# Kernel optimization log

Hardware: AMD Instinct MI355X
Metric: run time of the kernel (lower is better)

The kernel has to match this reference:

```python
import jax, jax.numpy as jnp
import numpy as np

HIDDEN = 1024
B, S = 32, 2048
MASKED_BIAS = -10000.0


def setup_inputs() -> dict:
    key = jax.random.key(0)
    ks = jax.random.split(key, 10)
    scale = 1.0 / np.sqrt(HIDDEN)
    inp = {
        "h": jax.random.normal(ks[0], (B, HIDDEN), jnp.float32),
        "K": jax.random.normal(ks[1], (B, S, HIDDEN), jnp.float32),
        "cov": jax.random.uniform(ks[2], (B, S), jnp.float32),
        "mask": jax.random.bernoulli(ks[3], 0.1, (B, S)).astype(jnp.float32),
        # parameters (PyTorch Linear: y = x @ W.T + b)
        "W_h": jax.random.uniform(ks[4], (HIDDEN, HIDDEN), jnp.float32, -scale, scale),
        "b_h": jnp.zeros((HIDDEN,), jnp.float32),
        "W_K": jax.random.uniform(ks[5], (HIDDEN, HIDDEN), jnp.float32, -scale, scale),
        "b_K": jnp.zeros((HIDDEN,), jnp.float32),
        "W_cov": jax.random.uniform(ks[6], (HIDDEN, 1), jnp.float32, -1.0, 1.0),
        "b_cov": jnp.zeros((HIDDEN,), jnp.float32),
        "W_v": jax.random.uniform(ks[7], (1, HIDDEN), jnp.float32, -scale, scale),
        "b_v": jnp.zeros((1,), jnp.float32),
    }
    return inp


def reference(h, K, cov, mask, W_h, b_h, W_K, b_K, W_cov, b_cov, W_v, b_v):
    # h_l: (B, 1, H); K_l: (B, S, H); c_l: (B, S, H)
    h_l = (h @ W_h.T + b_h)[:, None, :]
    K_l = jnp.einsum("bsh,gh->bsg", K, W_K) + b_K
    c_l = cov[:, :, None] * W_cov[:, 0] + b_cov  # linear_cov on scalar cov
    t = jnp.tanh(h_l + K_l + c_l)                 # (B, S, H)
    e = jnp.einsum("bsh,h->bs", t, W_v[0]) + b_v[0]
    e = e + mask * MASKED_BIAS
    a = jax.nn.softmax(e, axis=-1)                # (B, S)
    out = jnp.einsum("bs,bsh->bh", a, K)          # context vector
    cov_new = cov + a
    return (out, a, cov_new)
```

## Files before the change

kernel.cpp:

```cpp
#include <hip/hip_runtime.h>
#include <hip/hip_bf16.h>

#define HIDDEN 1024
#define B_SZ 32
#define S_SZ 2048
#define M_TOT (B_SZ * S_SZ)
#define MASKED_BIAS -10000.0f

using bf16   = __bf16;
using bf16x4 = __attribute__((ext_vector_type(4))) __bf16;
using bf16x8 = __attribute__((ext_vector_type(8))) __bf16;
using f32x4  = __attribute__((ext_vector_type(4))) float;

__device__ __forceinline__ float tanh_fast(float x) {
    float xc = fminf(fmaxf(x, -15.f), 15.f);
    float e2 = __expf(2.f * xc);
    return (e2 - 1.f) * __frcp_rn(e2 + 1.f);
}

__global__ __launch_bounds__(256) void k_wconv(
    const float* __restrict__ W, bf16* __restrict__ out)
{
    int i = blockIdx.x * 256 + threadIdx.x;
    const float4* p = (const float4*)W + (size_t)i * 2;
    float4 a = p[0], b = p[1];
    bf16x8 v = { (bf16)a.x, (bf16)a.y, (bf16)a.z, (bf16)a.w,
                 (bf16)b.x, (bf16)b.y, (bf16)b.z, (bf16)b.w };
    *(bf16x8*)(out + (size_t)i * 8) = v;
}

__global__ __launch_bounds__(256) void k_kconv(
    const float* __restrict__ K, bf16* __restrict__ out)
{
    size_t i = (size_t)blockIdx.x * 256 + threadIdx.x;
    const float4* p = (const float4*)K + i * 2;
    float4 a = p[0], b = p[1];
    bf16x8 v = { (bf16)a.x, (bf16)a.y, (bf16)a.z, (bf16)a.w,
                 (bf16)b.x, (bf16)b.y, (bf16)b.z, (bf16)b.w };
    *(bf16x8*)(out + i * 8) = v;
}

__global__ __launch_bounds__(256) void k_hlplus(
    const float* __restrict__ h, const float* __restrict__ W_h,
    const float* __restrict__ b_h, const float* __restrict__ b_K,
    const float* __restrict__ b_cov, float* __restrict__ hl_plus)
{
    int wid  = blockIdx.x * 4 + (threadIdx.x >> 6);
    int lane = threadIdx.x & 63;
    int b = wid & 31;
    int g = wid >> 5;
    const float4* hv = (const float4*)(h + b * HIDDEN);
    const float4* wv = (const float4*)(W_h + g * HIDDEN);
    float acc = 0.f;
#pragma unroll
    for (int i = 0; i < 4; ++i) {
        float4 a = hv[i * 64 + lane];
        float4 w = wv[i * 64 + lane];
        acc += a.x * w.x + a.y * w.y + a.z * w.z + a.w * w.w;
    }
#pragma unroll
    for (int off = 32; off; off >>= 1) acc += __shfl_xor(acc, off);
    if (lane == 0)
        hl_plus[b * HIDDEN + g] = acc + b_h[g] + b_K[g] + b_cov[g];
}

#define NT_N 4

__global__ __launch_bounds__(512) void k_fused_g(
    const bf16*  __restrict__ Kbf,
    const bf16*  __restrict__ Bbf,
    const float* __restrict__ hl_plus,
    const float* __restrict__ W_cov,
    const float* __restrict__ cov,
    const float* __restrict__ W_v,
    float* __restrict__ e_part)
{
    __shared__ __align__(16) bf16 AsT[2][2][256][32];
    __shared__ __align__(16) bf16 BsT[2][2][256][32];
    __shared__ float e_buf[256][4];

    const int tid = threadIdx.x;
    const int bid = blockIdx.x;
    const int lid = (bid & 7) * 128 + (bid >> 3);
    const int mt  = lid >> 2;
    const int nt  = lid & 3;
    const int row0 = mt * 256;
    const int col0 = nt * 256;

    const int w    = tid >> 6;
    const int lane = tid & 63;
    const int wr   = w >> 2;
    const int wc   = w & 3;
    const int lr   = lane & 15;
    const int kb   = lane >> 4;
    const int wrB  = wr * 128;
    const int wcB  = wc * 64;
    const int colA = (kb ^ ((lr >> 1) & 3)) * 8;

    const int srow = lane >> 2;
    const int gch  = (lane & 3) ^ ((lane >> 3) & 3);
    const bf16* Abase = Kbf + (size_t)(row0 + w * 32 + srow) * HIDDEN + gch * 8;
    const bf16* Bbase = Bbf + (size_t)(col0 + w * 32 + srow) * HIDDEN + gch * 8;

    f32x4 acc[8][4] = {};

#define STAGE(KT, H, D)                                                   \
    _Pragma("unroll") for (int j = 0; j < 2; ++j) {                       \
        __builtin_amdgcn_global_load_lds(                                 \
            (const __attribute__((address_space(1))) void*)               \
                (Abase + (size_t)j * 16 * HIDDEN + (KT) * 64 + (H) * 32), \
            (__attribute__((address_space(3))) void*)                     \
                &AsT[D][H][w * 32 + j * 16][0], 16, 0, 0);                \
        __builtin_amdgcn_global_load_lds(                                 \
            (const __attribute__((address_space(1))) void*)               \
                (Bbase + (size_t)j * 16 * HIDDEN + (KT) * 64 + (H) * 32), \
            (__attribute__((address_space(3))) void*)                     \
                &BsT[D][H][w * 32 + j * 16][0], 16, 0, 0);                \
    }

#define RD_A(D, H, MP)                                                   \
    _Pragma("unroll") for (int j = 0; j < 4; ++j)                        \
        afr[j] = *(const bf16x8*)                                        \
            &AsT[D][H][wrB + (MP) * 64 + j * 16 + lr][colA];

#define RD_B(D, H)                                                       \
    _Pragma("unroll") for (int n = 0; n < 4; ++n)                        \
        bfr[n] = *(const bf16x8*)&BsT[D][H][wcB + n * 16 + lr][colA];

#define MFMA16(MP)                                                       \
    __builtin_amdgcn_s_setprio(1);                                       \
    _Pragma("unroll") for (int j = 0; j < 4; ++j)                        \
        _Pragma("unroll") for (int n = 0; n < 4; ++n)                    \
            acc[(MP) * 4 + j][n] = __builtin_amdgcn_mfma_f32_16x16x32_bf16( \
                afr[j], bfr[n], acc[(MP) * 4 + j][n], 0, 0, 0);          \
    __builtin_amdgcn_s_setprio(0);

#define MEMBAR() asm volatile("" ::: "memory")
#define LGKM0()  asm volatile("s_waitcnt lgkmcnt(0)" ::: "memory")
#define VM(n)    asm volatile("s_waitcnt vmcnt(" #n ")" ::: "memory")
#define SBAR()   __builtin_amdgcn_s_barrier()
#define P_OPEN()  MEMBAR(); SBAR(); LGKM0();
#define P_CLOSE() MEMBAR(); SBAR();

#define TILE_STEADY(D, KT_NEXT)                                          \
    {                                                                    \
        bf16x8 afr[4], bfr[4];                                           \
        RD_B(D, 0) RD_A(D, 0, 0) STAGE(KT_NEXT, 0, D ^ 1)                \
        P_OPEN() MFMA16(0) P_CLOSE()                                     \
        RD_A(D, 0, 1)                                                    \
        P_OPEN() MFMA16(1) VM(4); P_CLOSE()                              \
        RD_B(D, 1) RD_A(D, 1, 0) STAGE(KT_NEXT, 1, D ^ 1)                \
        P_OPEN() MFMA16(0) P_CLOSE()                                     \
        RD_A(D, 1, 1)                                                    \
        P_OPEN() MFMA16(1) VM(4); P_CLOSE()                              \
    }

#define TILE_LAST(D)                                                     \
    {                                                                    \
        bf16x8 afr[4], bfr[4];                                           \
        RD_B(D, 0) RD_A(D, 0, 0)                                         \
        P_OPEN() MFMA16(0) P_CLOSE()                                     \
        RD_A(D, 0, 1)                                                    \
        P_OPEN() MFMA16(1) VM(0); P_CLOSE()                              \
        RD_B(D, 1) RD_A(D, 1, 0)                                         \
        P_OPEN() MFMA16(0) P_CLOSE()                                     \
        RD_A(D, 1, 1)                                                    \
        P_OPEN() MFMA16(1) P_CLOSE()                                     \
    }

    STAGE(0, 0, 0)
    STAGE(0, 1, 0)
    VM(4);
    MEMBAR(); SBAR();

    for (int kt2 = 0; kt2 < 7; ++kt2) {
        TILE_STEADY(0, 2 * kt2 + 1)
        TILE_STEADY(1, 2 * kt2 + 2)
    }
    TILE_STEADY(0, 15)
    TILE_LAST(1)

    const int bidx = row0 >> 11;
    float hlv[4], wcv[4], wvv[4];
#pragma unroll
    for (int n = 0; n < 4; ++n) {
        int g = col0 + wcB + n * 16 + lr;
        hlv[n] = hl_plus[bidx * HIDDEN + g];
        wcv[n] = W_cov[g];
        wvv[n] = W_v[g];
    }
#pragma unroll
    for (int am = 0; am < 8; ++am) {
#pragma unroll
        for (int i = 0; i < 4; ++i) {
            int rloc = wrB + am * 16 + kb * 4 + i;
            float cv = cov[row0 + rloc];
            float ep = 0.f;
#pragma unroll
            for (int n = 0; n < 4; ++n) {
                float arg = acc[am][n][i] + hlv[n] + cv * wcv[n];
                ep += tanh_fast(arg) * wvv[n];
            }
            ep += __shfl_xor(ep, 1);
            ep += __shfl_xor(ep, 2);
            ep += __shfl_xor(ep, 4);
            ep += __shfl_xor(ep, 8);
            if (lr == 0) e_buf[rloc][wc] = ep;
        }
    }
    __syncthreads();
    if (tid < 256)
        e_part[(size_t)nt * M_TOT + row0 + tid] =
            e_buf[tid][0] + e_buf[tid][1] + e_buf[tid][2] + e_buf[tid][3];

#undef STAGE
#undef RD_A
#undef RD_B
#undef MFMA16
#undef TILE_STEADY
#undef TILE_LAST
#undef MEMBAR
#undef LGKM0
#undef VM
#undef SBAR
#undef P_OPEN
#undef P_CLOSE
}

__global__ __launch_bounds__(256) void k_softmax(
    const float* __restrict__ e_part, const float* __restrict__ mask,
    const float* __restrict__ cov, const float* __restrict__ b_v,
    float* __restrict__ a_out, float* __restrict__ cov_out)
{
    __shared__ float red[8];
    int b = blockIdx.x, tid = threadIdx.x;
    float bv = b_v[0];
    float ev[8];
    float mx = -1e30f;
#pragma unroll
    for (int j = 0; j < 8; ++j) {
        int s = j * 256 + tid;
        int idx = b * S_SZ + s;
        float e = bv;
#pragma unroll
        for (int p = 0; p < 4; ++p) e += e_part[(size_t)p * M_TOT + idx];
        e += mask[idx] * MASKED_BIAS;
        ev[j] = e;
        mx = fmaxf(mx, e);
    }
#pragma unroll
    for (int off = 32; off; off >>= 1) mx = fmaxf(mx, __shfl_xor(mx, off));
    if ((tid & 63) == 0) red[tid >> 6] = mx;
    __syncthreads();
    mx = fmaxf(fmaxf(red[0], red[1]), fmaxf(red[2], red[3]));
    float sum = 0.f;
#pragma unroll
    for (int j = 0; j < 8; ++j) { ev[j] = __expf(ev[j] - mx); sum += ev[j]; }
#pragma unroll
    for (int off = 32; off; off >>= 1) sum += __shfl_xor(sum, off);
    if ((tid & 63) == 0) red[4 + (tid >> 6)] = sum;
    __syncthreads();
    sum = red[4] + red[5] + red[6] + red[7];
    float inv = 1.f / sum;
#pragma unroll
    for (int j = 0; j < 8; ++j) {
        int idx = b * S_SZ + j * 256 + tid;
        float a = ev[j] * inv;
        a_out[idx]   = a;
        cov_out[idx] = cov[idx] + a;
    }
}

__global__ __launch_bounds__(256) void k_ctx_part_bf(
    const bf16* __restrict__ Kbf, const float* __restrict__ a_out,
    float* __restrict__ part_out)
{
    int sc = blockIdx.x;
    int b  = blockIdx.y;
    int tid = threadIdx.x;
    const bf16* Kb = Kbf + ((size_t)b * S_SZ + sc * 128) * HIDDEN;
    const float* ab = a_out + b * S_SZ + sc * 128;
    float4 acc = {0.f, 0.f, 0.f, 0.f};
#pragma unroll 4
    for (int s = 0; s < 128; ++s) {
        float av = ab[s];
        bf16x4 kv = *(const bf16x4*)(Kb + (size_t)s * HIDDEN + tid * 4);
        acc.x += av * (float)kv[0];
        acc.y += av * (float)kv[1];
        acc.z += av * (float)kv[2];
        acc.w += av * (float)kv[3];
    }
    ((float4*)part_out)[((size_t)b * 16 + sc) * 256 + tid] = acc;
}

__global__ __launch_bounds__(256) void k_ctx_reduce(
    const float* __restrict__ part_out, float* __restrict__ out, int nc)
{
    int b = blockIdx.x, tid = threadIdx.x;
    float4 acc = {0.f, 0.f, 0.f, 0.f};
    for (int sc = 0; sc < nc; ++sc) {
        float4 v = ((const float4*)part_out)[((size_t)b * nc + sc) * 256 + tid];
        acc.x += v.x; acc.y += v.y; acc.z += v.z; acc.w += v.w;
    }
    ((float4*)out)[b * 256 + tid] = acc;
}

extern "C" void kernel_launch(void* const* d_in, const int* in_sizes, int n_in,
                              void* d_out, int out_size, void* d_ws, size_t ws_size,
                              hipStream_t stream)
{
    const float* h     = (const float*)d_in[0];
    const float* Kin   = (const float*)d_in[1];
    const float* cov   = (const float*)d_in[2];
    const float* mask  = (const float*)d_in[3];
    const float* W_h   = (const float*)d_in[4];
    const float* b_h   = (const float*)d_in[5];
    const float* W_K   = (const float*)d_in[6];
    const float* b_K   = (const float*)d_in[7];
    const float* W_cov = (const float*)d_in[8];
    const float* b_cov = (const float*)d_in[9];
    const float* W_v   = (const float*)d_in[10];
    const float* b_v   = (const float*)d_in[11];

    float* out_ctx = (float*)d_out;
    float* a_out   = out_ctx + B_SZ * HIDDEN;
    float* cov_out = a_out + M_TOT;

    float* ws       = (float*)d_ws;
    float* hl_plus  = ws;
    float* e_part   = ws + 32768;
    float* part_out = e_part;
    bf16*  Bbf      = (bf16*)(e_part + 4 * M_TOT);
    bf16*  Kbf      = (bf16*)((char*)Bbf + (size_t)HIDDEN * HIDDEN * sizeof(bf16));

    k_wconv<<<512, 256, 0, stream>>>(W_K, Bbf);
    k_hlplus<<<8192, 256, 0, stream>>>(h, W_h, b_h, b_K, b_cov, hl_plus);
    k_kconv<<<(M_TOT * HIDDEN / 8) / 256, 256, 0, stream>>>(Kin, Kbf);
    k_fused_g<<<256 * NT_N, 512, 0, stream>>>(
        Kbf, Bbf, hl_plus, W_cov, cov, W_v, e_part);
    k_softmax<<<B_SZ, 256, 0, stream>>>(e_part, mask, cov, b_v, a_out, cov_out);
    dim3 g4(16, B_SZ);
    k_ctx_part_bf<<<g4, 256, 0, stream>>>(Kbf, a_out, part_out);
    k_ctx_reduce<<<B_SZ, 256, 0, stream>>>(part_out, out_ctx, 16);
}
```

Before: 320.1 us.

## Shrink GEMM N-tile to 128 with K-step 32 and simpler double buffering

Replaces the 256x256 tile GEMM, which used a hand-scheduled barrier and waitcnt pipeline, with a 256x128 tile at K-step 32. The new version uses plain double buffering with __syncthreads and a launch bound of 4 waves per SIMD. The aim is lower LDS and register use so more blocks can be resident and hide latency. In exchange the K activations are re-read from memory twice as many times, with 8 column partials instead of 4. It also loses the fine-grained MFMA/load interleaving and adds more partial-sum traffic into softmax.

```diff
diff --git a/kernel.cpp b/kernel.cpp
--- a/kernel.cpp
+++ b/kernel.cpp
@@ -64,9 +64,9 @@
         hl_plus[b * HIDDEN + g] = acc + b_h[g] + b_K[g] + b_cov[g];
 }
 
-#define NT_N 4
-
-__global__ __launch_bounds__(512) void k_fused_g(
+#define NT_N 8
+
+__global__ __launch_bounds__(512, 4) void k_fused8(
     const bf16*  __restrict__ Kbf,
     const bf16*  __restrict__ Bbf,
     const float* __restrict__ hl_plus,
@@ -75,17 +75,17 @@
     const float* __restrict__ W_v,
     float* __restrict__ e_part)
 {
-    __shared__ __align__(16) bf16 AsT[2][2][256][32];
-    __shared__ __align__(16) bf16 BsT[2][2][256][32];
+    __shared__ __align__(16) bf16 As[2][256][32];
+    __shared__ __align__(16) bf16 Bs[2][128][32];
     __shared__ float e_buf[256][4];
 
     const int tid = threadIdx.x;
     const int bid = blockIdx.x;
-    const int lid = (bid & 7) * 128 + (bid >> 3);
-    const int mt  = lid >> 2;
-    const int nt  = lid & 3;
+    const int lid = (bid & 7) * 256 + (bid >> 3);
+    const int mt  = lid >> 3;
+    const int nt  = lid & 7;
     const int row0 = mt * 256;
-    const int col0 = nt * 256;
+    const int col0 = nt * 128;
 
     const int w    = tid >> 6;
     const int lane = tid & 63;
@@ -93,112 +93,82 @@
     const int wc   = w & 3;
     const int lr   = lane & 15;
     const int kb   = lane >> 4;
-    const int wrB  = wr * 128;
-    const int wcB  = wc * 64;
     const int colA = (kb ^ ((lr >> 1) & 3)) * 8;
 
     const int srow = lane >> 2;
     const int gch  = (lane & 3) ^ ((lane >> 3) & 3);
-    const bf16* Abase = Kbf + (size_t)(row0 + w * 32 + srow) * HIDDEN + gch * 8;
-    const bf16* Bbase = Bbf + (size_t)(col0 + w * 32 + srow) * HIDDEN + gch * 8;
-
-    f32x4 acc[8][4] = {};
-
-#define STAGE(KT, H, D)                                                   \
-    _Pragma("unroll") for (int j = 0; j < 2; ++j) {                       \
-        __builtin_amdgcn_global_load_lds(                                 \
-            (const __attribute__((address_space(1))) void*)               \
-                (Abase + (size_t)j * 16 * HIDDEN + (KT) * 64 + (H) * 32), \
-            (__attribute__((address_space(3))) void*)                     \
-                &AsT[D][H][w * 32 + j * 16][0], 16, 0, 0);                \
-        __builtin_amdgcn_global_load_lds(                                 \
-            (const __attribute__((address_space(1))) void*)               \
-                (Bbase + (size_t)j * 16 * HIDDEN + (KT) * 64 + (H) * 32), \
-            (__attribute__((address_space(3))) void*)                     \
-                &BsT[D][H][w * 32 + j * 16][0], 16, 0, 0);                \
-    }
-
-#define RD_A(D, H, MP)                                                   \
-    _Pragma("unroll") for (int j = 0; j < 4; ++j)                        \
-        afr[j] = *(const bf16x8*)                                        \
-            &AsT[D][H][wrB + (MP) * 64 + j * 16 + lr][colA];
-
-#define RD_B(D, H)                                                       \
-    _Pragma("unroll") for (int n = 0; n < 4; ++n)                        \
-        bfr[n] = *(const bf16x8*)&BsT[D][H][wcB + n * 16 + lr][colA];
-
-#define MFMA16(MP)                                                       \
-    __builtin_amdgcn_s_setprio(1);                                       \
-    _Pragma("unroll") for (int j = 0; j < 4; ++j)                        \
-        _Pragma("unroll") for (int n = 0; n < 4; ++n)                    \
-            acc[(MP) * 4 + j][n] = __builtin_amdgcn_mfma_f32_16x16x32_bf16( \
-                afr[j], bfr[n], acc[(MP) * 4 + j][n], 0, 0, 0);          \
-    __builtin_amdgcn_s_setprio(0);
-
-#define MEMBAR() asm volatile("" ::: "memory")
-#define LGKM0()  asm volatile("s_waitcnt lgkmcnt(0)" ::: "memory")
-#define VM(n)    asm volatile("s_waitcnt vmcnt(" #n ")" ::: "memory")
-#define SBAR()   __builtin_amdgcn_s_barrier()
-#define P_OPEN()  MEMBAR(); SBAR(); LGKM0();
-#define P_CLOSE() MEMBAR(); SBAR();
-
-#define TILE_STEADY(D, KT_NEXT)                                          \
-    {                                                                    \
-        bf16x8 afr[4], bfr[4];                                           \
-        RD_B(D, 0) RD_A(D, 0, 0) STAGE(KT_NEXT, 0, D ^ 1)                \
-        P_OPEN() MFMA16(0) P_CLOSE()                                     \
-        RD_A(D, 0, 1)                                                    \
-        P_OPEN() MFMA16(1) VM(4); P_CLOSE()                              \
-        RD_B(D, 1) RD_A(D, 1, 0) STAGE(KT_NEXT, 1, D ^ 1)                \
-        P_OPEN() MFMA16(0) P_CLOSE()                                     \
-        RD_A(D, 1, 1)                                                    \
-        P_OPEN() MFMA16(1) VM(4); P_CLOSE()                              \
-    }
-
-#define TILE_LAST(D)                                                     \
-    {                                                                    \
-        bf16x8 afr[4], bfr[4];                                           \
-        RD_B(D, 0) RD_A(D, 0, 0)                                         \
-        P_OPEN() MFMA16(0) P_CLOSE()                                     \
-        RD_A(D, 0, 1)                                                    \
-        P_OPEN() MFMA16(1) VM(0); P_CLOSE()                              \
-        RD_B(D, 1) RD_A(D, 1, 0)                                         \
-        P_OPEN() MFMA16(0) P_CLOSE()                                     \
-        RD_A(D, 1, 1)                                                    \
-        P_OPEN() MFMA16(1) P_CLOSE()                                     \
-    }
-
-    STAGE(0, 0, 0)
-    STAGE(0, 1, 0)
-    VM(4);
-    MEMBAR(); SBAR();
-
-    for (int kt2 = 0; kt2 < 7; ++kt2) {
-        TILE_STEADY(0, 2 * kt2 + 1)
-        TILE_STEADY(1, 2 * kt2 + 2)
-    }
-    TILE_STEADY(0, 15)
-    TILE_LAST(1)
+    const bf16* Abase = Kbf + (size_t)(row0 + w * 16 + srow) * HIDDEN + gch * 8;
+    const bf16* Bbase = Bbf + (size_t)(col0 + w * 16 + srow) * HIDDEN + gch * 8;
+
+    f32x4 acc[8][2] = {};
+
+#define STAGE(KT, BUF)                                                    \
+    __builtin_amdgcn_global_load_lds(                                     \
+        (const __attribute__((address_space(1))) void*)(Abase + (KT) * 32),\
+        (__attribute__((address_space(3))) void*)&As[BUF][w * 16][0],     \
+        16, 0, 0);                                                        \
+    __builtin_amdgcn_global_load_lds(                                     \
+        (const __attribute__((address_space(1))) void*)                   \
+            (Abase + (size_t)128 * HIDDEN + (KT) * 32),                   \
+        (__attribute__((address_space(3))) void*)&As[BUF][128 + w * 16][0],\
+        16, 0, 0);                                                        \
+    __builtin_amdgcn_global_load_lds(                                     \
+        (const __attribute__((address_space(1))) void*)(Bbase + (KT) * 32),\
+        (__attribute__((address_space(3))) void*)&Bs[BUF][w * 16][0],     \
+        16, 0, 0);
+
+#define TILE_COMPUTE(BUF)                                                 \
+    {                                                                     \
+        bf16x8 afr[8], bfr[2];                                            \
+        _Pragma("unroll") for (int j = 0; j < 8; ++j)                     \
+            afr[j] = *(const bf16x8*)                                     \
+                &As[BUF][wr * 128 + j * 16 + lr][colA];                   \
+        _Pragma("unroll") for (int n = 0; n < 2; ++n)                     \
+            bfr[n] = *(const bf16x8*)&Bs[BUF][wc * 32 + n * 16 + lr][colA];\
+        __builtin_amdgcn_s_setprio(1);                                    \
+        _Pragma("unroll") for (int j = 0; j < 8; ++j)                     \
+            _Pragma("unroll") for (int n = 0; n < 2; ++n)                 \
+                acc[j][n] = __builtin_amdgcn_mfma_f32_16x16x32_bf16(      \
+                    afr[j], bfr[n], acc[j][n], 0, 0, 0);                  \
+        __builtin_amdgcn_s_setprio(0);                                    \
+    }
+
+    STAGE(0, 0)
+    __syncthreads();
+
+    for (int i = 0; i < 15; ++i) {
+        const int t = i * 2;
+        STAGE(t + 1, 1)
+        TILE_COMPUTE(0)
+        __syncthreads();
+        STAGE(t + 2, 0)
+        TILE_COMPUTE(1)
+        __syncthreads();
+    }
+    STAGE(31, 1)
+    TILE_COMPUTE(0)
+    __syncthreads();
+    TILE_COMPUTE(1)
 
     const int bidx = row0 >> 11;
-    float hlv[4], wcv[4], wvv[4];
-#pragma unroll
-    for (int n = 0; n < 4; ++n) {
-        int g = col0 + wcB + n * 16 + lr;
+    float hlv[2], wcv[2], wvv[2];
+#pragma unroll
+    for (int n = 0; n < 2; ++n) {
+        int g = col0 + wc * 32 + n * 16 + lr;
         hlv[n] = hl_plus[bidx * HIDDEN + g];
         wcv[n] = W_cov[g];
         wvv[n] = W_v[g];
     }
 #pragma unroll
-    for (int am = 0; am < 8; ++am) {
+    for (int j = 0; j < 8; ++j) {
 #pragma unroll
         for (int i = 0; i < 4; ++i) {
-            int rloc = wrB + am * 16 + kb * 4 + i;
+            int rloc = wr * 128 + j * 16 + kb * 4 + i;
             float cv = cov[row0 + rloc];
             float ep = 0.f;
 #pragma unroll
-            for (int n = 0; n < 4; ++n) {
-                float arg = acc[am][n][i] + hlv[n] + cv * wcv[n];
+            for (int n = 0; n < 2; ++n) {
+                float arg = acc[j][n][i] + hlv[n] + cv * wcv[n];
                 ep += tanh_fast(arg) * wvv[n];
             }
             ep += __shfl_xor(ep, 1);
@@ -214,17 +184,7 @@
             e_buf[tid][0] + e_buf[tid][1] + e_buf[tid][2] + e_buf[tid][3];
 
 #undef STAGE
-#undef RD_A
-#undef RD_B
-#undef MFMA16
-#undef TILE_STEADY
-#undef TILE_LAST
-#undef MEMBAR
-#undef LGKM0
-#undef VM
-#undef SBAR
-#undef P_OPEN
-#undef P_CLOSE
+#undef TILE_COMPUTE
 }
 
 __global__ __launch_bounds__(256) void k_softmax(
@@ -243,7 +203,7 @@
         int idx = b * S_SZ + s;
         float e = bv;
 #pragma unroll
-        for (int p = 0; p < 4; ++p) e += e_part[(size_t)p * M_TOT + idx];
+        for (int p = 0; p < 8; ++p) e += e_part[(size_t)p * M_TOT + idx];
         e += mask[idx] * MASKED_BIAS;
         ev[j] = e;
         mx = fmaxf(mx, e);
@@ -330,13 +290,13 @@
     float* hl_plus  = ws;
     float* e_part   = ws + 32768;
     float* part_out = e_part;
-    bf16*  Bbf      = (bf16*)(e_part + 4 * M_TOT);
+    bf16*  Bbf      = (bf16*)(e_part + 8 * M_TOT);
     bf16*  Kbf      = (bf16*)((char*)Bbf + (size_t)HIDDEN * HIDDEN * sizeof(bf16));
 
     k_wconv<<<512, 256, 0, stream>>>(W_K, Bbf);
     k_hlplus<<<8192, 256, 0, stream>>>(h, W_h, b_h, b_K, b_cov, hl_plus);
     k_kconv<<<(M_TOT * HIDDEN / 8) / 256, 256, 0, stream>>>(Kin, Kbf);
-    k_fused_g<<<256 * NT_N, 512, 0, stream>>>(
+    k_fused8<<<256 * NT_N, 512, 0, stream>>>(
         Kbf, Bbf, hl_plus, W_cov, cov, W_v, e_part);
     k_softmax<<<B_SZ, 256, 0, stream>>>(e_part, mask, cov, b_v, a_out, cov_out);
     dim3 g4(16, B_SZ);
```

After: 301.6 us. 5.8% less time.
